# Kernel tuning notes

Hardware: AMD Instinct MI355X
Metric: run time of the kernel (lower is better)

## Reference

```python
import jax, jax.numpy as jnp
import numpy as np

DIM = 1024
MULTIPLE_OF = 256
NUM_EXPERTS = 8
TOP_K = 2
T = 2048  # flattened tokens


def _hidden_dim(dim: int, multiple_of: int) -> int:
    h = 4 * dim
    h = int(2 * h / 3)
    return multiple_of * ((h + multiple_of - 1) // multiple_of)

HIDDEN = _hidden_dim(DIM, MULTIPLE_OF)  # 2816


def setup_inputs() -> dict:
    key = jax.random.key(0)
    k_x, k_idx, k1, k2, k3 = jax.random.split(key, 5)
    x = jax.random.normal(k_x, (T, DIM), dtype=jnp.float32)
    expert_indices = jax.random.randint(k_idx, (T, TOP_K), 0, NUM_EXPERTS, dtype=jnp.int32)
    # parameters, matching nn.Parameter(torch.randn(E, H, D))
    w1 = jax.random.normal(k1, (NUM_EXPERTS, HIDDEN, DIM), dtype=jnp.float32)
    w2 = jax.random.normal(k2, (NUM_EXPERTS, HIDDEN, DIM), dtype=jnp.float32)
    w3 = jax.random.normal(k3, (NUM_EXPERTS, HIDDEN, DIM), dtype=jnp.float32)
    return {"x": x, "expert_indices": expert_indices, "w1": w1, "w2": w2, "w3": w3}


def reference(x, expert_indices, w1, w2, w3):
    # Same math as the torch module, but instead of materializing the
    # per-token gathered weights [T, A, H, D] (which the original does and
    # which blows up memory), we compute the SwiGLU FFN for ALL experts via
    # dense GEMMs and gather the selected experts' outputs per token.
    # Gather commutes with the per-expert linear maps, so math is identical.
    x1_all = jax.nn.silu(jnp.einsum('td,ehd->teh', x, w1))  # [T, E, H]
    x3_all = jnp.einsum('td,ehd->teh', x, w3)               # [T, E, H]
    g_all = x1_all * x3_all                                  # [T, E, H]
    out_all = jnp.einsum('teh,ehd->ted', g_all, w2)          # [T, E, D]
    # select top_k experts per token -> [T, A, D]
    idx = expert_indices[:, :, None].astype(jnp.int32)       # [T, A, 1]
    return jnp.take_along_axis(out_all, idx, axis=1)
```

## Files before the change

### kernel.cpp

```cpp
#include <hip/hip_runtime.h>

#define NTOK 2048
#define NEXP 8
#define TOPK 2
#define NITEM 4096
#define DIM 1024
#define HID 2816
#define CAP 4096
#define LDP 72

typedef unsigned short u16;
typedef __bf16 bf16x8 __attribute__((ext_vector_type(8)));
typedef float f32x4 __attribute__((ext_vector_type(4)));

__device__ __forceinline__ u16 f2bf(float f) {
  unsigned u = __float_as_uint(f);
  return (u16)((u + 0x7FFFu + ((u >> 16) & 1u)) >> 16);
}
__device__ __forceinline__ unsigned pk2(float a, float b) {
  return (unsigned)f2bf(a) | ((unsigned)f2bf(b) << 16);
}
__device__ __forceinline__ void async16(const void* g, void* l) {
  __builtin_amdgcn_global_load_lds(
      (const __attribute__((address_space(1))) unsigned int*)g,
      (__attribute__((address_space(3))) unsigned int*)l, 16, 0, 0);
}
__device__ __forceinline__ const bf16x8* fragpA(const u16* base, int row, int ko) {
  int byte = ((row << 7) + (ko << 1)) ^ ((row & 7) << 4);
  return (const bf16x8*)((const char*)base + byte);
}
__device__ __forceinline__ const bf16x8* fragpB(const u16* base, int row, int kg) {
  int byte = (row << 6) + ((kg << 4) ^ (((row >> 1) & 3) << 4));
  return (const bf16x8*)((const char*)base + byte);
}
__device__ __forceinline__ void cvst8(const float4& a, const float4& b, void* dst) {
  union { __bf16 h[8]; uint4 q; } u;
  u.h[0] = (__bf16)a.x; u.h[1] = (__bf16)a.y; u.h[2] = (__bf16)a.z; u.h[3] = (__bf16)a.w;
  u.h[4] = (__bf16)b.x; u.h[5] = (__bf16)b.y; u.h[6] = (__bf16)b.z; u.h[7] = (__bf16)b.w;
  *(uint4*)dst = u.q;
}

__global__ void zero8(int* counts) {
  if (threadIdx.x < NEXP) counts[threadIdx.x] = 0;
}

__global__ void bucket(const int* __restrict__ ei, int* counts, int* lists) {
  int item = blockIdx.x * 256 + threadIdx.x;
  if (item < NITEM) {
    int e = ei[item] & 7;
    int pos = atomicAdd(&counts[e], 1);
    if (pos < CAP) lists[e * CAP + pos] = item;
  }
}

__global__ __launch_bounds__(256) void cvt8(const float* __restrict__ src,
                                            u16* __restrict__ dst, int n8) {
  int i = blockIdx.x * 256 + threadIdx.x;
  if (i >= n8) return;
  float4 v0 = *(const float4*)(src + (size_t)i * 8);
  float4 v1 = *(const float4*)(src + (size_t)i * 8 + 4);
  uint4 u;
  u.x = pk2(v0.x, v0.y); u.y = pk2(v0.z, v0.w);
  u.z = pk2(v1.x, v1.y); u.w = pk2(v1.z, v1.w);
  *(uint4*)(dst + (size_t)i * 8) = u;
}


__global__ __launch_bounds__(256, 2) void gemm1I(
    const u16* __restrict__ xb, const float* __restrict__ w1,
    const float* __restrict__ w3, const int* __restrict__ counts,
    const int* __restrict__ lists, u16* __restrict__ G) {
  __shared__ __align__(16) u16 As[3][256 * 32];
  __shared__ __align__(16) u16 B1s[2][64 * 32];
  __shared__ __align__(16) u16 B3s[2][64 * 32];
  __shared__ int toks[256];

  const int flat = blockIdx.x;
  const int n_id = flat % 44;
  const int t2 = flat / 44;
  const int e = t2 & 7;
  const int m_id = t2 >> 3;

  int cnt = counts[e];
  if ((unsigned)cnt > CAP) cnt = 0;
  const int m0 = m_id * 256;
  if (m0 >= cnt) return;
  const int n0 = n_id * 64;
  const int tid = threadIdx.x;

  {
    int r = m0 + tid;
    int it = lists[e * CAP + (r < cnt ? r : 0)];
    toks[tid] = ((unsigned)it < NITEM) ? it : 0;
  }
  __syncthreads();

  const int lane = tid & 63;
  const int wrow = (tid >> 6) * 64;
  const int lr = lane & 15;
  const int kg = lane >> 4;

  const int prow = tid >> 2;
  const int q = tid & 3;
  const int ascol = (q ^ ((prow >> 1) & 3)) * 8;
  const u16* xs[4];
#pragma unroll
  for (int p = 0; p < 4; ++p)
    xs[p] = xb + (size_t)(toks[p * 64 + prow] >> 1) * DIM + ascol;

  const int br = prow;
  const float* w1p = w1 + ((size_t)e * HID + n0 + br) * DIM + q * 8;
  const float* w3p = w3 + ((size_t)e * HID + n0 + br) * DIM + q * 8;
  const int bby = (br << 6) + ((q << 4) ^ (((br >> 1) & 3) << 4));

  float4 b1r[2][2], b3r[2][2];
  f32x4 acc1[4][4] = {};
  f32x4 acc3[4][4] = {};

#define KCL(k) ((k) < DIM ? (k) : (DIM - 32))
#define G1_LOADB(set, k)                                  \
  {                                                       \
    b1r[set][0] = *(const float4*)(w1p + (k));            \
    b1r[set][1] = *(const float4*)(w1p + (k) + 4);        \
    b3r[set][0] = *(const float4*)(w3p + (k));            \
    b3r[set][1] = *(const float4*)(w3p + (k) + 4);        \
  }
#define G1_STGA(buf, k)                                   \
  {                                                       \
    char* aD = (char*)As[buf] + tid * 16;                 \
    async16(xs[0] + (k), aD);                             \
    async16(xs[1] + (k), aD + 4096);                      \
    async16(xs[2] + (k), aD + 8192);                      \
    async16(xs[3] + (k), aD + 12288);                     \
  }
#define G1_WRITEB(buf, set)                                   \
  {                                                           \
    cvst8(b1r[set][0], b1r[set][1], (char*)B1s[buf] + bby);   \
    cvst8(b3r[set][0], b3r[set][1], (char*)B3s[buf] + bby);   \
  }
#define G1_COMP(ab, bb)                                                      \
  {                                                                          \
    bf16x8 a[4];                                                             \
    _Pragma("unroll") for (int m = 0; m < 4; ++m)                            \
        a[m] = *fragpB(As[ab], wrow + m * 16 + lr, kg);                      \
    _Pragma("unroll") for (int n = 0; n < 4; ++n) {                          \
      bf16x8 b1 = *fragpB(B1s[bb], n * 16 + lr, kg);                         \
      bf16x8 b3 = *fragpB(B3s[bb], n * 16 + lr, kg);                         \
      _Pragma("unroll") for (int m = 0; m < 4; ++m) {                        \
        acc1[m][n] = __builtin_amdgcn_mfma_f32_16x16x32_bf16(a[m], b1, acc1[m][n], 0, 0, 0); \
        acc3[m][n] = __builtin_amdgcn_mfma_f32_16x16x32_bf16(a[m], b3, acc3[m][n], 0, 0, 0); \
      }                                                                      \
    }                                                                        \
  }
#define G1_ITER(I, AC, AS2, BC, BW)                                  \
  {                                                                  \
    G1_STGA(AS2, KCL(32 * ((I) + 2)));                               \
    __builtin_amdgcn_sched_barrier(0);                               \
    asm volatile("s_waitcnt vmcnt(4)" ::: "memory");                 \
    __builtin_amdgcn_sched_barrier(0);                               \
    G1_WRITEB(BW, BW);                                               \
    G1_LOADB(BC, KCL(32 * ((I) + 2)));                               \
    __builtin_amdgcn_sched_barrier(0);                               \
    G1_COMP(AC, BC);                                                 \
    asm volatile("s_waitcnt lgkmcnt(0)" ::: "memory");               \
    __builtin_amdgcn_sched_barrier(0);                               \
    __builtin_amdgcn_s_barrier();                                    \
    __builtin_amdgcn_sched_barrier(0);                               \
  }

  G1_LOADB(0, 0);
  G1_STGA(0, 0);
  G1_LOADB(1, 32);
  G1_STGA(1, 32);
  __builtin_amdgcn_sched_barrier(0);
  asm volatile("s_waitcnt vmcnt(8)" ::: "memory");
  __builtin_amdgcn_sched_barrier(0);
  G1_WRITEB(0, 0);
  asm volatile("s_waitcnt lgkmcnt(0)" ::: "memory");
  __builtin_amdgcn_sched_barrier(0);
  __builtin_amdgcn_s_barrier();
  __builtin_amdgcn_sched_barrier(0);

  for (int i = 0; i < 30; i += 6) {
    G1_ITER(i + 0, 0, 2, 0, 1);
    G1_ITER(i + 1, 1, 0, 1, 0);
    G1_ITER(i + 2, 2, 1, 0, 1);
    G1_ITER(i + 3, 0, 2, 1, 0);
    G1_ITER(i + 4, 1, 0, 0, 1);
    G1_ITER(i + 5, 2, 1, 1, 0);
  }
  G1_ITER(30, 0, 2, 0, 1);
  G1_ITER(31, 1, 0, 1, 0);
#undef G1_ITER
#undef G1_COMP
#undef G1_WRITEB
#undef G1_STGA
#undef G1_LOADB
#undef KCL

#pragma unroll
  for (int m = 0; m < 4; ++m) {
#pragma unroll
    for (int r = 0; r < 4; ++r) {
      const int row = wrow + m * 16 + kg * 4 + r;
      if (m0 + row < cnt) {
        const int it = toks[row];
        u16* gp = G + (size_t)it * HID + n0 + lr;
#pragma unroll
        for (int n = 0; n < 4; ++n) {
          float v1 = acc1[m][n][r];
          float v3 = acc3[m][n][r];
          float s = v1 / (1.f + __expf(-v1)) * v3;
          gp[n * 16] = f2bf(s);
        }
      }
    }
  }
}

__global__ __launch_bounds__(256, 1) void gemm2T(
    const u16* __restrict__ G, const float* __restrict__ w2,
    const int* __restrict__ counts, const int* __restrict__ lists,
    float* __restrict__ out) {
  __shared__ __align__(16) u16 As[2][256 * 64];
  __shared__ __align__(16) u16 Bs[2][64 * 64];
  __shared__ int toks[256];

  const int flat = blockIdx.x;
  const int n_id = flat & 15;
  const int t2 = flat >> 4;
  const int e = t2 & 7;
  const int m_id = t2 >> 3;

  int cnt = counts[e];
  if ((unsigned)cnt > CAP) cnt = 0;
  const int m0 = m_id * 256;
  if (m0 >= cnt) return;
  const int n0 = n_id * 64;
  const int tid = threadIdx.x;

  {
    int r = m0 + tid;
    int it = lists[e * CAP + (r < cnt ? r : 0)];
    toks[tid] = ((unsigned)it < NITEM) ? it : 0;
  }
  __syncthreads();

  const int lane = tid & 63;
  const int wrow = (tid >> 6) * 64;
  const int lr = lane & 15;
  const int kg = lane >> 4;

  const int srow = tid >> 3;
  const int c = tid & 7;
  const int scol = ((c ^ (srow & 7)) * 8);
  const u16* as[8];
#pragma unroll
  for (int p = 0; p < 8; ++p)
    as[p] = G + (size_t)toks[p * 32 + srow] * HID + scol;

  const int h = tid & 63;
  const int tg = tid >> 6;
  const float* w2p = w2 + ((size_t)e * HID + h) * DIM + n0 + tg * 4;

  float4 bq[2][4];
  f32x4 acc[4][4] = {};

#define KCL2(k) ((k) < HID ? (k) : (HID - 64))
#define G2_LOADB(set, k)                                           \
  {                                                                \
    _Pragma("unroll") for (int qq = 0; qq < 4; ++qq)               \
        bq[set][qq] = *(const float4*)(w2p + (size_t)(k) * DIM + qq * 16); \
  }
#define G2_STGA(buf, k)                                            \
  {                                                                \
    char* aD = (char*)As[buf] + tid * 16;                          \
    _Pragma("unroll") for (int p = 0; p < 8; ++p)                  \
        async16(as[p] + (k), aD + p * 4096);                       \
  }
#define G2_WB1(buf, set, qq, jj, val)                                        \
  {                                                                          \
    int d_ = tg * 4 + (qq) * 16 + (jj);                                      \
    int by_ = ((d_ << 7) + (h << 1)) ^ ((d_ & 7) << 4);                      \
    *(u16*)((char*)Bs[buf] + by_) = f2bf(val);                               \
  }
#define G2_WRITEB(buf, set)                                  \
  {                                                          \
    _Pragma("unroll") for (int qq = 0; qq < 4; ++qq) {       \
      G2_WB1(buf, set, qq, 0, bq[set][qq].x);                \
      G2_WB1(buf, set, qq, 1, bq[set][qq].y);                \
      G2_WB1(buf, set, qq, 2, bq[set][qq].z);                \
      G2_WB1(buf, set, qq, 3, bq[set][qq].w);                \
    }                                                        \
  }
#define G2_COMP(cb)                                                          \
  {                                                                          \
    _Pragma("unroll") for (int kk = 0; kk < 2; ++kk) {                       \
      const int ko = kk * 32 + kg * 8;                                       \
      bf16x8 a[4], b[4];                                                     \
      _Pragma("unroll") for (int m = 0; m < 4; ++m)                          \
          a[m] = *fragpA(As[cb], wrow + m * 16 + lr, ko);                    \
      _Pragma("unroll") for (int n = 0; n < 4; ++n)                          \
          b[n] = *fragpA(Bs[cb], n * 16 + lr, ko);                           \
      _Pragma("unroll") for (int n = 0; n < 4; ++n)                          \
          _Pragma("unroll") for (int m = 0; m < 4; ++m)                      \
              acc[m][n] = __builtin_amdgcn_mfma_f32_16x16x32_bf16(a[m], b[n], acc[m][n], 0, 0, 0); \
    }                                                                        \
  }
#define G2_IT(I, PB, CB)                                             \
  {                                                                  \
    G2_STGA(PB, KCL2(64 * ((I) + 1)));                               \
    __builtin_amdgcn_sched_barrier(0);                               \
    asm volatile("s_waitcnt vmcnt(8)" ::: "memory");                 \
    __builtin_amdgcn_sched_barrier(0);                               \
    G2_WRITEB(PB, PB);                                               \
    G2_LOADB(CB, KCL2(64 * ((I) + 2)));                              \
    __builtin_amdgcn_sched_barrier(0);                               \
    G2_COMP(CB);                                                     \
    asm volatile("s_waitcnt vmcnt(4) lgkmcnt(0)" ::: "memory");      \
    __builtin_amdgcn_sched_barrier(0);                               \
    __builtin_amdgcn_s_barrier();                                    \
    __builtin_amdgcn_sched_barrier(0);                               \
  }

  G2_LOADB(0, 0);
  G2_STGA(0, 0);
  G2_LOADB(1, 64);
  __builtin_amdgcn_sched_barrier(0);
  asm volatile("s_waitcnt vmcnt(4)" ::: "memory");
  __builtin_amdgcn_sched_barrier(0);
  G2_WRITEB(0, 0);
  asm volatile("s_waitcnt lgkmcnt(0)" ::: "memory");
  __builtin_amdgcn_sched_barrier(0);
  __builtin_amdgcn_s_barrier();
  __builtin_amdgcn_sched_barrier(0);

  for (int i = 0; i < 44; i += 2) {
    G2_IT(i, 1, 0);
    G2_IT(i + 1, 0, 1);
  }
#undef G2_IT
#undef G2_COMP
#undef G2_WRITEB
#undef G2_WB1
#undef G2_STGA
#undef G2_LOADB
#undef KCL2

#pragma unroll
  for (int m = 0; m < 4; ++m) {
#pragma unroll
    for (int r = 0; r < 4; ++r) {
      const int row = wrow + m * 16 + kg * 4 + r;
      if (m0 + row < cnt) {
        const int it = toks[row];
        float* op = out + (size_t)it * DIM + n0 + lr;
#pragma unroll
        for (int n = 0; n < 4; ++n)
          op[n * 16] = acc[m][n][r];
      }
    }
  }
}


__global__ __launch_bounds__(256, 2) void gemm1B(
    const float* __restrict__ x, const float* __restrict__ w1,
    const float* __restrict__ w3, const int* __restrict__ counts,
    const int* __restrict__ lists, u16* __restrict__ G) {
  __shared__ __align__(16) u16 As[128 * LDP];
  __shared__ __align__(16) u16 B1s[128 * LDP];
  __shared__ __align__(16) u16 B3s[128 * LDP];
  __shared__ int toks[128];

  const int e = blockIdx.z;
  int cnt = counts[e];
  if ((unsigned)cnt > CAP) cnt = 0;
  const int m0 = blockIdx.y * 128;
  if (m0 >= cnt) return;
  const int n0 = blockIdx.x * 128;
  const int tid = threadIdx.x;

  if (tid < 128) {
    int r = m0 + tid;
    int it = lists[e * CAP + (r < cnt ? r : 0)];
    toks[tid] = ((unsigned)it < NITEM) ? it : 0;
  }
  __syncthreads();

  const int lane = tid & 63;
  const int wr = ((tid >> 7) & 1) * 64;
  const int wc = ((tid >> 6) & 1) * 64;
  const int lr = lane & 15;
  const int kg = lane >> 4;
  const int arow = tid >> 3;
  const int c8 = (tid & 7) * 8;

  const float* xsrc[4];
#pragma unroll
  for (int p = 0; p < 4; ++p)
    xsrc[p] = x + (size_t)(toks[p * 32 + arow] >> 1) * DIM + c8;
  const float* w1p = w1 + ((size_t)e * HID + n0 + arow) * DIM + c8;
  const float* w3p = w3 + ((size_t)e * HID + n0 + arow) * DIM + c8;

  f32x4 acc1[4][4] = {};
  f32x4 acc3[4][4] = {};

  for (int k0 = 0; k0 < DIM; k0 += 64) {
#pragma unroll
    for (int p = 0; p < 4; ++p) {
      float4 v0 = *(const float4*)(xsrc[p] + k0);
      float4 v1 = *(const float4*)(xsrc[p] + k0 + 4);
      uint4 u;
      u.x = pk2(v0.x, v0.y); u.y = pk2(v0.z, v0.w);
      u.z = pk2(v1.x, v1.y); u.w = pk2(v1.z, v1.w);
      *(uint4*)&As[(p * 32 + arow) * LDP + c8] = u;
    }
#pragma unroll
    for (int p = 0; p < 4; ++p) {
      float4 v0 = *(const float4*)(w1p + (size_t)(p * 32) * DIM + k0);
      float4 v1 = *(const float4*)(w1p + (size_t)(p * 32) * DIM + k0 + 4);
      uint4 u;
      u.x = pk2(v0.x, v0.y); u.y = pk2(v0.z, v0.w);
      u.z = pk2(v1.x, v1.y); u.w = pk2(v1.z, v1.w);
      *(uint4*)&B1s[(p * 32 + arow) * LDP + c8] = u;
      v0 = *(const float4*)(w3p + (size_t)(p * 32) * DIM + k0);
      v1 = *(const float4*)(w3p + (size_t)(p * 32) * DIM + k0 + 4);
      u.x = pk2(v0.x, v0.y); u.y = pk2(v0.z, v0.w);
      u.z = pk2(v1.x, v1.y); u.w = pk2(v1.z, v1.w);
      *(uint4*)&B3s[(p * 32 + arow) * LDP + c8] = u;
    }
    __syncthreads();
#pragma unroll
    for (int kk = 0; kk < 2; ++kk) {
      const int ko = kk * 32 + kg * 8;
      bf16x8 a[4];
#pragma unroll
      for (int m = 0; m < 4; ++m)
        a[m] = *(const bf16x8*)&As[(wr + m * 16 + lr) * LDP + ko];
#pragma unroll
      for (int n = 0; n < 4; ++n) {
        bf16x8 b1 = *(const bf16x8*)&B1s[(wc + n * 16 + lr) * LDP + ko];
        bf16x8 b3 = *(const bf16x8*)&B3s[(wc + n * 16 + lr) * LDP + ko];
#pragma unroll
        for (int m = 0; m < 4; ++m) {
          acc1[m][n] = __builtin_amdgcn_mfma_f32_16x16x32_bf16(a[m], b1, acc1[m][n], 0, 0, 0);
          acc3[m][n] = __builtin_amdgcn_mfma_f32_16x16x32_bf16(a[m], b3, acc3[m][n], 0, 0, 0);
        }
      }
    }
    __syncthreads();
  }

#pragma unroll
  for (int m = 0; m < 4; ++m) {
#pragma unroll
    for (int r = 0; r < 4; ++r) {
      const int row = wr + m * 16 + kg * 4 + r;
      if (m0 + row < cnt) {
        const int it = toks[row];
        u16* gp = G + (size_t)it * HID + n0 + wc + lr;
#pragma unroll
        for (int n = 0; n < 4; ++n) {
          float v1 = acc1[m][n][r];
          float v3 = acc3[m][n][r];
          float s = v1 / (1.f + __expf(-v1)) * v3;
          gp[n * 16] = f2bf(s);
        }
      }
    }
  }
}

__global__ __launch_bounds__(256, 2) void gemm2B(
    const u16* __restrict__ G, const float* __restrict__ w2,
    const int* __restrict__ counts, const int* __restrict__ lists,
    float* __restrict__ out) {
  __shared__ __align__(16) u16 As[128 * LDP];
  __shared__ __align__(16) u16 Bs[128 * LDP];
  __shared__ int toks[128];

  const int e = blockIdx.z;
  int cnt = counts[e];
  if ((unsigned)cnt > CAP) cnt = 0;
  const int m0 = blockIdx.y * 128;
  if (m0 >= cnt) return;
  const int n0 = blockIdx.x * 128;
  const int tid = threadIdx.x;

  if (tid < 128) {
    int r = m0 + tid;
    int it = lists[e * CAP + (r < cnt ? r : 0)];
    toks[tid] = ((unsigned)it < NITEM) ? it : 0;
  }
  __syncthreads();

  const int lane = tid & 63;
  const int wr = ((tid >> 7) & 1) * 64;
  const int wc = ((tid >> 6) & 1) * 64;
  const int lr = lane & 15;
  const int kg = lane >> 4;
  const int arow = tid >> 3;
  const int c8 = (tid & 7) * 8;
  const int brow = tid >> 5;
  const int d4 = (tid & 31) * 4;

  const u16* asrc[4];
#pragma unroll
  for (int p = 0; p < 4; ++p)
    asrc[p] = G + (size_t)toks[p * 32 + arow] * HID + c8;
  const float* bsrc = w2 + ((size_t)e * HID) * DIM + n0 + d4;

  f32x4 acc[4][4] = {};

  for (int k0 = 0; k0 < HID; k0 += 64) {
#pragma unroll
    for (int p = 0; p < 4; ++p) {
      uint4 u = *(const uint4*)(asrc[p] + k0);
      *(uint4*)&As[(p * 32 + arow) * LDP + c8] = u;
    }
#pragma unroll
    for (int p = 0; p < 8; ++p) {
      const int hl = p * 8 + brow;
      float4 v = *(const float4*)(bsrc + (size_t)(k0 + hl) * DIM);
      Bs[(d4 + 0) * LDP + hl] = f2bf(v.x);
      Bs[(d4 + 1) * LDP + hl] = f2bf(v.y);
      Bs[(d4 + 2) * LDP + hl] = f2bf(v.z);
      Bs[(d4 + 3) * LDP + hl] = f2bf(v.w);
    }
    __syncthreads();
#pragma unroll
    for (int kk = 0; kk < 2; ++kk) {
      const int ko = kk * 32 + kg * 8;
      bf16x8 a[4];
#pragma unroll
      for (int m = 0; m < 4; ++m)
        a[m] = *(const bf16x8*)&As[(wr + m * 16 + lr) * LDP + ko];
#pragma unroll
      for (int n = 0; n < 4; ++n) {
        bf16x8 b = *(const bf16x8*)&Bs[(wc + n * 16 + lr) * LDP + ko];
#pragma unroll
        for (int m = 0; m < 4; ++m)
          acc[m][n] = __builtin_amdgcn_mfma_f32_16x16x32_bf16(a[m], b, acc[m][n], 0, 0, 0);
      }
    }
    __syncthreads();
  }

#pragma unroll
  for (int m = 0; m < 4; ++m) {
#pragma unroll
    for (int r = 0; r < 4; ++r) {
      const int row = wr + m * 16 + kg * 4 + r;
      if (m0 + row < cnt) {
        const int it = toks[row];
        float* op = out + (size_t)it * DIM + n0 + wc + lr;
#pragma unroll
        for (int n = 0; n < 4; ++n)
          op[n * 16] = acc[m][n][r];
      }
    }
  }
}

extern "C" void kernel_launch(void* const* d_in, const int* in_sizes, int n_in,
                              void* d_out, int out_size, void* d_ws, size_t ws_size,
                              hipStream_t stream) {
  (void)in_sizes; (void)n_in; (void)out_size;
  const float* x  = (const float*)d_in[0];
  const int*   ei = (const int*)d_in[1];
  const float* w1 = (const float*)d_in[2];
  const float* w2 = (const float*)d_in[3];
  const float* w3 = (const float*)d_in[4];
  float* out = (float*)d_out;

  char* ws = (char*)d_ws;

  const size_t oG = 0;
  const size_t oXB = 23068672u;
  const size_t oCNT = oXB + 4194304u;
  const size_t oLST = oCNT + 64u;
  const size_t needA = oLST + 131072u;

  if (ws_size >= needA) {
    u16* G      = (u16*)(ws + oG);
    u16* xb     = (u16*)(ws + oXB);
    int* counts = (int*)(ws + oCNT);
    int* lists  = (int*)(ws + oLST);

    zero8<<<1, 64, 0, stream>>>(counts);
    bucket<<<NITEM / 256, 256, 0, stream>>>(ei, counts, lists);
    cvt8<<<(NTOK * DIM / 8) / 256, 256, 0, stream>>>(x, xb, NTOK * DIM / 8);
    gemm1I<<<44 * 8 * 16, 256, 0, stream>>>(xb, w1, w3, counts, lists, G);
    gemm2T<<<16 * 8 * 16, 256, 0, stream>>>(G, w2, counts, lists, out);
  } else {
    u16* G      = (u16*)ws;
    int* counts = (int*)(ws + 23068672u);
    int* lists  = (int*)(ws + 23068736u);

    zero8<<<1, 64, 0, stream>>>(counts);
    bucket<<<NITEM / 256, 256, 0, stream>>>(ei, counts, lists);
    gemm1B<<<dim3(HID / 128, CAP / 128, NEXP), 256, 0, stream>>>(x, w1, w3, counts, lists, G);
    gemm2B<<<dim3(DIM / 128, CAP / 128, NEXP), 256, 0, stream>>>(G, w2, counts, lists, out);
  }
}
```

Baseline: 247.7 us.

## Double-buffer gemm1 A tiles and shrink gemm2 M-tile for occupancy

gemm1's three-stage A pipeline becomes a two-buffer ping-pong. The A prefetch and B write move to the start of each iteration, and the wait counts change to match. gemm2T cuts its M tile from 256 to 128 rows and spreads the four waves over a 2x2 layout (64x32 per wave). It doubles the grid and raises launch bounds to 3 blocks per CU so more blocks run at once. The trade-off is less prefetch depth in gemm1 and less weight reuse per block in gemm2, since each w2 tile is reloaded for twice as many row blocks.

Result: faster. 223.9 us (-9.6%).

```diff
diff --git a/kernel.cpp b/kernel.cpp
--- a/kernel.cpp
+++ b/kernel.cpp
@@ -66,11 +66,11 @@
 }
 
 
-__global__ __launch_bounds__(256, 2) void gemm1I(
+__global__ __launch_bounds__(256, 2) void gemm1H(
     const u16* __restrict__ xb, const float* __restrict__ w1,
     const float* __restrict__ w3, const int* __restrict__ counts,
     const int* __restrict__ lists, u16* __restrict__ G) {
-  __shared__ __align__(16) u16 As[3][256 * 32];
+  __shared__ __align__(16) u16 As[2][256 * 32];
   __shared__ __align__(16) u16 B1s[2][64 * 32];
   __shared__ __align__(16) u16 B3s[2][64 * 32];
   __shared__ int toks[256];
@@ -138,42 +138,40 @@
     cvst8(b1r[set][0], b1r[set][1], (char*)B1s[buf] + bby);   \
     cvst8(b3r[set][0], b3r[set][1], (char*)B3s[buf] + bby);   \
   }
-#define G1_COMP(ab, bb)                                                      \
+#define G1_COMP(cb)                                                          \
   {                                                                          \
     bf16x8 a[4];                                                             \
     _Pragma("unroll") for (int m = 0; m < 4; ++m)                            \
-        a[m] = *fragpB(As[ab], wrow + m * 16 + lr, kg);                      \
+        a[m] = *fragpB(As[cb], wrow + m * 16 + lr, kg);                      \
     _Pragma("unroll") for (int n = 0; n < 4; ++n) {                          \
-      bf16x8 b1 = *fragpB(B1s[bb], n * 16 + lr, kg);                         \
-      bf16x8 b3 = *fragpB(B3s[bb], n * 16 + lr, kg);                         \
+      bf16x8 b1 = *fragpB(B1s[cb], n * 16 + lr, kg);                         \
+      bf16x8 b3 = *fragpB(B3s[cb], n * 16 + lr, kg);                         \
       _Pragma("unroll") for (int m = 0; m < 4; ++m) {                        \
         acc1[m][n] = __builtin_amdgcn_mfma_f32_16x16x32_bf16(a[m], b1, acc1[m][n], 0, 0, 0); \
         acc3[m][n] = __builtin_amdgcn_mfma_f32_16x16x32_bf16(a[m], b3, acc3[m][n], 0, 0, 0); \
       }                                                                      \
     }                                                                        \
   }
-#define G1_ITER(I, AC, AS2, BC, BW)                                  \
+#define G1_ITER(i, cb)                                               \
   {                                                                  \
-    G1_STGA(AS2, KCL(32 * ((I) + 2)));                               \
-    __builtin_amdgcn_sched_barrier(0);                               \
-    asm volatile("s_waitcnt vmcnt(4)" ::: "memory");                 \
-    __builtin_amdgcn_sched_barrier(0);                               \
-    G1_WRITEB(BW, BW);                                               \
-    G1_LOADB(BC, KCL(32 * ((I) + 2)));                               \
-    __builtin_amdgcn_sched_barrier(0);                               \
-    G1_COMP(AC, BC);                                                 \
-    asm volatile("s_waitcnt lgkmcnt(0)" ::: "memory");               \
+    G1_STGA(cb ^ 1, KCL(32 * ((i) + 1)));                            \
+    G1_WRITEB(cb ^ 1, cb ^ 1);              \
+    __builtin_amdgcn_sched_barrier(0);                               \
+    G1_LOADB(cb, KCL(32 * ((i) + 2)));                               \
+    __builtin_amdgcn_sched_barrier(0);                               \
+    G1_COMP(cb);                                                     \
+    asm volatile("s_waitcnt vmcnt(4) lgkmcnt(0)" ::: "memory");      \
     __builtin_amdgcn_sched_barrier(0);                               \
     __builtin_amdgcn_s_barrier();                                    \
     __builtin_amdgcn_sched_barrier(0);                               \
   }
 
   G1_LOADB(0, 0);
+  __builtin_amdgcn_sched_barrier(0);
   G1_STGA(0, 0);
+  __builtin_amdgcn_sched_barrier(0);
   G1_LOADB(1, 32);
-  G1_STGA(1, 32);
-  __builtin_amdgcn_sched_barrier(0);
-  asm volatile("s_waitcnt vmcnt(8)" ::: "memory");
+  asm volatile("s_waitcnt vmcnt(4)" ::: "memory");
   __builtin_amdgcn_sched_barrier(0);
   G1_WRITEB(0, 0);
   asm volatile("s_waitcnt lgkmcnt(0)" ::: "memory");
@@ -181,16 +179,10 @@
   __builtin_amdgcn_s_barrier();
   __builtin_amdgcn_sched_barrier(0);
 
-  for (int i = 0; i < 30; i += 6) {
-    G1_ITER(i + 0, 0, 2, 0, 1);
-    G1_ITER(i + 1, 1, 0, 1, 0);
-    G1_ITER(i + 2, 2, 1, 0, 1);
-    G1_ITER(i + 3, 0, 2, 1, 0);
-    G1_ITER(i + 4, 1, 0, 0, 1);
-    G1_ITER(i + 5, 2, 1, 1, 0);
-  }
-  G1_ITER(30, 0, 2, 0, 1);
-  G1_ITER(31, 1, 0, 1, 0);
+  for (int i = 0; i < 32; i += 2) {
+    G1_ITER(i, 0);
+    G1_ITER(i + 1, 1);
+  }
 #undef G1_ITER
 #undef G1_COMP
 #undef G1_WRITEB
@@ -218,13 +210,13 @@
   }
 }
 
-__global__ __launch_bounds__(256, 1) void gemm2T(
+__global__ __launch_bounds__(256, 3) void gemm2T(
     const u16* __restrict__ G, const float* __restrict__ w2,
     const int* __restrict__ counts, const int* __restrict__ lists,
     float* __restrict__ out) {
-  __shared__ __align__(16) u16 As[2][256 * 64];
+  __shared__ __align__(16) u16 As[2][128 * 64];
   __shared__ __align__(16) u16 Bs[2][64 * 64];
-  __shared__ int toks[256];
+  __shared__ int toks[128];
 
   const int flat = blockIdx.x;
   const int n_id = flat & 15;
@@ -234,12 +226,12 @@
 
   int cnt = counts[e];
   if ((unsigned)cnt > CAP) cnt = 0;
-  const int m0 = m_id * 256;
+  const int m0 = m_id * 128;
   if (m0 >= cnt) return;
   const int n0 = n_id * 64;
   const int tid = threadIdx.x;
 
-  {
+  if (tid < 128) {
     int r = m0 + tid;
     int it = lists[e * CAP + (r < cnt ? r : 0)];
     toks[tid] = ((unsigned)it < NITEM) ? it : 0;
@@ -247,16 +239,18 @@
   __syncthreads();
 
   const int lane = tid & 63;
-  const int wrow = (tid >> 6) * 64;
+  const int wid = tid >> 6;
+  const int wr = (wid >> 1) * 64;
+  const int wc = (wid & 1) * 32;
   const int lr = lane & 15;
   const int kg = lane >> 4;
 
   const int srow = tid >> 3;
   const int c = tid & 7;
   const int scol = ((c ^ (srow & 7)) * 8);
-  const u16* as[8];
-#pragma unroll
-  for (int p = 0; p < 8; ++p)
+  const u16* as[4];
+#pragma unroll
+  for (int p = 0; p < 4; ++p)
     as[p] = G + (size_t)toks[p * 32 + srow] * HID + scol;
 
   const int h = tid & 63;
@@ -264,7 +258,7 @@
   const float* w2p = w2 + ((size_t)e * HID + h) * DIM + n0 + tg * 4;
 
   float4 bq[2][4];
-  f32x4 acc[4][4] = {};
+  f32x4 acc[4][2] = {};
 
 #define KCL2(k) ((k) < HID ? (k) : (HID - 64))
 #define G2_LOADB(set, k)                                           \
@@ -275,10 +269,10 @@
 #define G2_STGA(buf, k)                                            \
   {                                                                \
     char* aD = (char*)As[buf] + tid * 16;                          \
-    _Pragma("unroll") for (int p = 0; p < 8; ++p)                  \
+    _Pragma("unroll") for (int p = 0; p < 4; ++p)                  \
         async16(as[p] + (k), aD + p * 4096);                       \
   }
-#define G2_WB1(buf, set, qq, jj, val)                                        \
+#define G2_WB1(buf, qq, jj, val)                                             \
   {                                                                          \
     int d_ = tg * 4 + (qq) * 16 + (jj);                                      \
     int by_ = ((d_ << 7) + (h << 1)) ^ ((d_ & 7) << 4);                      \
@@ -287,22 +281,22 @@
 #define G2_WRITEB(buf, set)                                  \
   {                                                          \
     _Pragma("unroll") for (int qq = 0; qq < 4; ++qq) {       \
-      G2_WB1(buf, set, qq, 0, bq[set][qq].x);                \
-      G2_WB1(buf, set, qq, 1, bq[set][qq].y);                \
-      G2_WB1(buf, set, qq, 2, bq[set][qq].z);                \
-      G2_WB1(buf, set, qq, 3, bq[set][qq].w);                \
+      G2_WB1(buf, qq, 0, bq[set][qq].x);                     \
+      G2_WB1(buf, qq, 1, bq[set][qq].y);                     \
+      G2_WB1(buf, qq, 2, bq[set][qq].z);                     \
+      G2_WB1(buf, qq, 3, bq[set][qq].w);                     \
     }                                                        \
   }
 #define G2_COMP(cb)                                                          \
   {                                                                          \
     _Pragma("unroll") for (int kk = 0; kk < 2; ++kk) {                       \
       const int ko = kk * 32 + kg * 8;                                       \
-      bf16x8 a[4], b[4];                                                     \
+      bf16x8 a[4], b[2];                                                     \
       _Pragma("unroll") for (int m = 0; m < 4; ++m)                          \
-          a[m] = *fragpA(As[cb], wrow + m * 16 + lr, ko);                    \
-      _Pragma("unroll") for (int n = 0; n < 4; ++n)                          \
-          b[n] = *fragpA(Bs[cb], n * 16 + lr, ko);                           \
-      _Pragma("unroll") for (int n = 0; n < 4; ++n)                          \
+          a[m] = *fragpA(As[cb], wr + m * 16 + lr, ko);                      \
+      _Pragma("unroll") for (int n = 0; n < 2; ++n)                          \
+          b[n] = *fragpA(Bs[cb], wc + n * 16 + lr, ko);                      \
+      _Pragma("unroll") for (int n = 0; n < 2; ++n)                          \
           _Pragma("unroll") for (int m = 0; m < 4; ++m)                      \
               acc[m][n] = __builtin_amdgcn_mfma_f32_16x16x32_bf16(a[m], b[n], acc[m][n], 0, 0, 0); \
     }                                                                        \
@@ -311,7 +305,7 @@
   {                                                                  \
     G2_STGA(PB, KCL2(64 * ((I) + 1)));                               \
     __builtin_amdgcn_sched_barrier(0);                               \
-    asm volatile("s_waitcnt vmcnt(8)" ::: "memory");                 \
+    asm volatile("s_waitcnt vmcnt(4)" ::: "memory");                 \
     __builtin_amdgcn_sched_barrier(0);                               \
     G2_WRITEB(PB, PB);                                               \
     G2_LOADB(CB, KCL2(64 * ((I) + 2)));                              \
@@ -351,12 +345,12 @@
   for (int m = 0; m < 4; ++m) {
 #pragma unroll
     for (int r = 0; r < 4; ++r) {
-      const int row = wrow + m * 16 + kg * 4 + r;
+      const int row = wr + m * 16 + kg * 4 + r;
       if (m0 + row < cnt) {
         const int it = toks[row];
-        float* op = out + (size_t)it * DIM + n0 + lr;
-#pragma unroll
-        for (int n = 0; n < 4; ++n)
+        float* op = out + (size_t)it * DIM + n0 + wc + lr;
+#pragma unroll
+        for (int n = 0; n < 2; ++n)
           op[n * 16] = acc[m][n][r];
       }
     }
@@ -591,8 +585,8 @@
     zero8<<<1, 64, 0, stream>>>(counts);
     bucket<<<NITEM / 256, 256, 0, stream>>>(ei, counts, lists);
     cvt8<<<(NTOK * DIM / 8) / 256, 256, 0, stream>>>(x, xb, NTOK * DIM / 8);
-    gemm1I<<<44 * 8 * 16, 256, 0, stream>>>(xb, w1, w3, counts, lists, G);
-    gemm2T<<<16 * 8 * 16, 256, 0, stream>>>(G, w2, counts, lists, out);
+    gemm1H<<<44 * 8 * 16, 256, 0, stream>>>(xb, w1, w3, counts, lists, G);
+    gemm2T<<<16 * 8 * 32, 256, 0, stream>>>(G, w2, counts, lists, out);
   } else {
     u16* G      = (u16*)ws;
     int* counts = (int*)(ws + 23068672u);
```
